# Performance work log

Measured on AMD Instinct MI355X. Metric: run time of the kernel, lower is better.

## Reference

```python
import jax, jax.numpy as jnp
import numpy as np

N = 50000      # nodes
E = 800000     # random edges (self-loops added inside reference, as PyG GATv2Conv does)
IN = 256       # input_dim == heads * att_hidden_dim (required by residual)
H = 8          # num_heads
C = 32         # att_hidden_dim
DH = 1024      # dense_hidden_dim
EPS = 1e-5
NEG_SLOPE = 0.2


def setup_inputs() -> dict:
    key = jax.random.key(0)
    ks = jax.random.split(key, 8)
    s = 0.05
    return {
        "x": jax.random.normal(ks[0], (N, IN), jnp.float32),
        "edge_index": jax.random.randint(ks[1], (2, E), 0, N, dtype=jnp.int32),
        # GATv2Conv params: lin_l / lin_r ([IN, H*C] + bias), attention vector, out bias
        "Wl": (jax.random.normal(ks[2], (IN, H * C), jnp.float32) * s),
        "bl": jnp.zeros((H * C,), jnp.float32),
        "Wr": (jax.random.normal(ks[3], (IN, H * C), jnp.float32) * s),
        "br": jnp.zeros((H * C,), jnp.float32),
        "att": (jax.random.normal(ks[4], (H, C), jnp.float32) * s),
        "b_gat": jnp.zeros((H * C,), jnp.float32),
        # LayerNorm 1 (PyG graph-mode) affine params
        "g1": jnp.ones((H * C,), jnp.float32),
        "be1": jnp.zeros((H * C,), jnp.float32),
        # MLP: dense_2 (H*C -> DH), dense_3 (DH -> IN)
        "W2": (jax.random.normal(ks[5], (H * C, DH), jnp.float32) * s),
        "b2": jnp.zeros((DH,), jnp.float32),
        "W3": (jax.random.normal(ks[6], (DH, IN), jnp.float32) * s),
        "b3": jnp.zeros((IN,), jnp.float32),
        # LayerNorm 3 affine params
        "g3": jnp.ones((IN,), jnp.float32),
        "be3": jnp.zeros((IN,), jnp.float32),
    }


def graph_layernorm(x, g, b):
    # torch_geometric.nn.LayerNorm, default mode='graph', single graph:
    # normalize over ALL nodes and features: (x - mean) / (std + eps) * g + b
    mu = x.mean()
    xc = x - mu
    std = jnp.sqrt((xc * xc).mean())
    return (xc / (std + EPS)) * g + b


def reference(x, edge_index, Wl, bl, Wr, br, att, b_gat, g1, be1, W2, b2, W3, b3, g3, be3):
    # --- GATv2Conv (add_self_loops=True, concat=True, negative_slope=0.2) ---
    loops = jnp.arange(N, dtype=edge_index.dtype)
    src = jnp.concatenate([edge_index[0], loops])  # message sources j
    dst = jnp.concatenate([edge_index[1], loops])  # message targets i

    xl = (x @ Wl + bl).reshape(N, H, C)  # source-side transform (lin_l)
    xr = (x @ Wr + br).reshape(N, H, C)  # target-side transform (lin_r)

    # per-edge GATv2 attention: leaky_relu(x_l[j] + x_r[i]) . att
    e = jax.nn.leaky_relu(xl[src] + xr[dst], NEG_SLOPE)   # [E+N, H, C]
    logits = jnp.einsum('ehc,hc->eh', e, att)             # [E+N, H]

    # segment softmax over incoming edges of each target node
    m = jax.ops.segment_max(logits, dst, num_segments=N)  # [N, H]
    p = jnp.exp(logits - m[dst])
    denom = jax.ops.segment_sum(p, dst, num_segments=N)   # [N, H]
    alpha = p / denom[dst]                                # [E+N, H]

    # scatter-add weighted source features
    agg = jax.ops.segment_sum(alpha[:, :, None] * xl[src], dst, num_segments=N)
    gat_out = agg.reshape(N, H * C) + b_gat               # concat heads + bias

    # --- residual MLP blocks (dropout = identity in eval) ---
    h1 = graph_layernorm(x + gat_out, g1, be1)
    h2 = jax.nn.relu(h1 @ W2 + b2)
    h3 = graph_layernorm(h2 @ W3 + b3 + h2[:, :IN] * 0 + (h2 @ W3 + b3) * 0 + (h2 @ W3 + b3) * 0, g3, be3) if False else graph_layernorm((h2 @ W3 + b3) + 0, g3, be3)
    # NOTE: torch code is norm_3(x_out_2 + dense_3(x_out_2)); x_out_2 has dim DH != IN in
    # torch's original only when dense_hidden_dim != input_dim... faithful version below:
    h3 = graph_layernorm(h2 @ W3 + b3, g3, be3)
    return h3
```

## Files before the change

kernel.cpp:

```cpp
#include <hip/hip_runtime.h>
#include <hip/hip_bf16.h>

#define HC 256
#define DHID 1024
#define LN_EPS 1e-5f
#define NSLOT 1024

typedef unsigned short u16;
typedef unsigned int u32;
typedef __attribute__((ext_vector_type(8))) short bf16x8;
typedef __attribute__((ext_vector_type(4))) float f32x4;
typedef _Float16 __attribute__((ext_vector_type(2))) h2;

__device__ __forceinline__ float bf2f(u16 u) {
  union { u32 i; float f; } v; v.i = ((u32)u) << 16; return v.f;
}
__device__ __forceinline__ u16 f2bf(float f) {
  union { float f; u32 i; } v; v.f = f;
  u32 r = v.i + 0x7fffu + ((v.i >> 16) & 1u);
  return (u16)(r >> 16);
}
__device__ __forceinline__ u16 f2h(float f) {
  union { _Float16 h; u16 u; } v; v.h = (_Float16)f; return v.u;
}
__device__ __forceinline__ float dot2(h2 a, h2 b, float c) {
  return __builtin_amdgcn_fdot2(a, b, c, false);
}
__device__ __forceinline__ void gload16(const u16* g, u16* ldsbase, int byteoff) {
  __builtin_amdgcn_global_load_lds(
      (const __attribute__((address_space(1))) void*)g,
      (__attribute__((address_space(3))) void*)((char*)ldsbase + byteoff),
      16, 0, 0);
}

template<bool RELU, int OMODE>
__global__ __launch_bounds__(256, 4) void gemm_mfma(
    const u16* __restrict__ Ab, const u16* __restrict__ BT,
    const float* __restrict__ bias,
    void* __restrict__ outp, double* __restrict__ sl,
    int M, int K, int NB)
{
  __shared__ __align__(16) u16 Asm[128 * 64];
  __shared__ __align__(16) u16 Bsm[128 * 64];
  const int tid = threadIdx.x;
  const int wid = tid >> 6, lane = tid & 63;
  const int rowBase = blockIdx.x * 128;
  const int colBase = blockIdx.y * 128;
  const int wr = (wid >> 1) * 64, wc = (wid & 1) * 64;
  const int ccol = lane & 15, g = lane >> 4;
  f32x4 acc[4][4] = {};
  const int nt = K >> 6;

  for (int t = 0; t < nt; ++t) {
    const int k0 = t << 6;
#pragma unroll
    for (int s = 0; s < 4; ++s) {
      const int L = s * 256 + tid;
      const int r = L >> 3;
      const int gc = ((L & 7) ^ (r & 7)) << 3;
      int gr = rowBase + r; gr = gr < M ? gr : M - 1;
      const int lb = __builtin_amdgcn_readfirstlane(s * 4096 + wid * 1024);
      gload16(&Ab[(size_t)gr * K + k0 + gc], Asm, lb);
    }
#pragma unroll
    for (int s = 0; s < 4; ++s) {
      const int L = s * 256 + tid;
      const int r = L >> 3;
      const int gc = ((L & 7) ^ (r & 7)) << 3;
      const int lb = __builtin_amdgcn_readfirstlane(s * 4096 + wid * 1024);
      gload16(&BT[(size_t)(colBase + r) * K + k0 + gc], Bsm, lb);
    }
    __syncthreads();
#pragma unroll
    for (int kk = 0; kk < 2; ++kk) {
      bf16x8 af[4], bfr[4];
      const int q = kk * 4 + g;
#pragma unroll
      for (int mr = 0; mr < 4; ++mr) {
        const int row = wr + mr * 16 + ccol;
        af[mr] = *(const bf16x8*)&Asm[(row << 6) + ((q ^ (row & 7)) << 3)];
      }
#pragma unroll
      for (int nc = 0; nc < 4; ++nc) {
        const int row = wc + nc * 16 + ccol;
        bfr[nc] = *(const bf16x8*)&Bsm[(row << 6) + ((q ^ (row & 7)) << 3)];
      }
#pragma unroll
      for (int mr = 0; mr < 4; ++mr)
#pragma unroll
        for (int nc = 0; nc < 4; ++nc)
          acc[mr][nc] = __builtin_amdgcn_mfma_f32_16x16x32_bf16(af[mr], bfr[nc], acc[mr][nc], 0, 0, 0);
    }
    __syncthreads();
  }

  u16* ob = (u16*)outp;
  float* of = (float*)outp;
  const int crow = g * 4;
  float s1 = 0.f, s2 = 0.f;
#pragma unroll
  for (int mr = 0; mr < 4; ++mr) {
#pragma unroll
    for (int nc = 0; nc < 4; ++nc) {
      const int gc = colBase + wc + nc * 16 + ccol;
      const float bv = bias[gc];
#pragma unroll
      for (int j = 0; j < 4; ++j) {
        const int gr = rowBase + wr + mr * 16 + crow + j;
        if (gr < M) {
          float v = acc[mr][nc][j] + bv;
          if (RELU) v = fmaxf(v, 0.f);
          if (OMODE == 1) {
            ob[(size_t)gr * NB + gc] = f2bf(v);
          } else if (OMODE == 2) {
            ob[(size_t)gr * NB + gc] = f2h(v);
          } else {
            of[(size_t)gr * NB + gc] = v;
            s1 += v; s2 += v * v;
          }
        }
      }
    }
  }
  if (OMODE == 0) {
#pragma unroll
    for (int d = 1; d < 64; d <<= 1) {
      s1 += __shfl_xor(s1, d);
      s2 += __shfl_xor(s2, d);
    }
    if (lane == 0) {
      int slot = ((blockIdx.x + blockIdx.y * 397) * 4 + wid) & (NSLOT - 1);
      atomicAdd(&sl[slot * 2 + 0], (double)s1);
      atomicAdd(&sl[slot * 2 + 1], (double)s2);
    }
  }
}

__global__ __launch_bounds__(256) void xcvt(const float* __restrict__ x,
                                            u16* __restrict__ xb, long n8) {
  for (long i = blockIdx.x * (long)blockDim.x + threadIdx.x; i < n8;
       i += (long)gridDim.x * blockDim.x) {
    const float* p = &x[i * 8];
    float4 f0 = *(const float4*)p;
    float4 f1 = *(const float4*)(p + 4);
    bf16x8 v;
    v[0] = (short)f2bf(f0.x); v[1] = (short)f2bf(f0.y);
    v[2] = (short)f2bf(f0.z); v[3] = (short)f2bf(f0.w);
    v[4] = (short)f2bf(f1.x); v[5] = (short)f2bf(f1.y);
    v[6] = (short)f2bf(f1.z); v[7] = (short)f2bf(f1.w);
    *(bf16x8*)&xb[i * 8] = v;
  }
}

__global__ __launch_bounds__(256) void transpose_all(
    const float* __restrict__ Wl, const float* __restrict__ Wr,
    const float* __restrict__ W2, const float* __restrict__ W3,
    u16* __restrict__ WT1, u16* __restrict__ W2T, u16* __restrict__ W3T)
{
  __shared__ float T[32][33];
  int b = blockIdx.x;
  const float* W; u16* WT; int K, NB, kb;
  if (b < 64)       { W = Wl; WT = WT1;              K = 256;  NB = 256;  kb = 8; }
  else if (b < 128) { W = Wr; WT = WT1 + 65536;      K = 256;  NB = 256;  kb = 8;  b -= 64; }
  else if (b < 384) { W = W2; WT = W2T;              K = 256;  NB = 1024; kb = 8;  b -= 128; }
  else              { W = W3; WT = W3T;              K = 1024; NB = 256;  kb = 32; b -= 384; }
  const int k0 = (b % kb) * 32, n0 = (b / kb) * 32;
  const int tx = threadIdx.x & 31, ty = threadIdx.x >> 5;
#pragma unroll
  for (int i = 0; i < 32; i += 8)
    T[ty + i][tx] = W[(size_t)(k0 + ty + i) * NB + n0 + tx];
  __syncthreads();
#pragma unroll
  for (int i = 0; i < 32; i += 8)
    WT[(size_t)(n0 + ty + i) * K + k0 + tx] = f2bf(T[tx][ty + i]);
}

__global__ __launch_bounds__(256) void w2scale(u16* __restrict__ W2T,
                                               const float* __restrict__ A1c) {
  const int i = blockIdx.x * blockDim.x + threadIdx.x;
  const int kb = (i & 31) << 3;
  bf16x8 v = *(bf16x8*)&W2T[(size_t)i * 8];
  float4 a0 = *(const float4*)&A1c[kb];
  float4 a1 = *(const float4*)&A1c[kb + 4];
  bf16x8 w;
  w[0] = (short)f2bf(bf2f((u16)v[0]) * a0.x);
  w[1] = (short)f2bf(bf2f((u16)v[1]) * a0.y);
  w[2] = (short)f2bf(bf2f((u16)v[2]) * a0.z);
  w[3] = (short)f2bf(bf2f((u16)v[3]) * a0.w);
  w[4] = (short)f2bf(bf2f((u16)v[4]) * a1.x);
  w[5] = (short)f2bf(bf2f((u16)v[5]) * a1.y);
  w[6] = (short)f2bf(bf2f((u16)v[6]) * a1.z);
  w[7] = (short)f2bf(bf2f((u16)v[7]) * a1.w);
  *(bf16x8*)&W2T[(size_t)i * 8] = w;
}

__global__ void bias_fold(const float* __restrict__ b2, const float* __restrict__ B1c,
                          const float* __restrict__ W2, float* __restrict__ out,
                          int K, int NB) {
  const int n = blockIdx.x * blockDim.x + threadIdx.x;
  if (n < NB) {
    float s = b2[n];
    for (int k = 0; k < K; ++k) s = fmaf(B1c[k], W2[(size_t)k * NB + n], s);
    out[n] = s;
  }
}

__global__ void deg_count(const int* __restrict__ dst, int* __restrict__ deg, int E) {
  int i = blockIdx.x * blockDim.x + threadIdx.x;
  if (i < E) atomicAdd(&deg[dst[i]], 1);
}

__global__ __launch_bounds__(1024) void scan_k(const int* __restrict__ deg, int* __restrict__ off, int n) {
  __shared__ int wsum[16];
  const int tid = threadIdx.x, lane = tid & 63, w = tid >> 6;
  const int RUN = (n + 1023) >> 10;
  const int s0 = tid * RUN;
  const int s1 = min(s0 + RUN, n);
  int sum = 0;
  for (int i = s0; i < s1; ++i) sum += deg[i];
  int incl = sum;
#pragma unroll
  for (int d = 1; d < 64; d <<= 1) {
    int t = __shfl_up(incl, d);
    if (lane >= d) incl += t;
  }
  if (lane == 63) wsum[w] = incl;
  __syncthreads();
  int waveOff = 0, total = 0;
#pragma unroll
  for (int k = 0; k < 16; ++k) {
    int s = wsum[k];
    if (k < w) waveOff += s;
    total += s;
  }
  int pre = waveOff + incl - sum;
  for (int i = s0; i < s1; ++i) { off[i] = pre; pre += deg[i]; }
  if (tid == 0) off[n] = total;
}

__global__ void fill_csr(const int* __restrict__ src, const int* __restrict__ dst,
                         const int* __restrict__ off, int* __restrict__ cur,
                         int* __restrict__ csr, int E) {
  int i = blockIdx.x * blockDim.x + threadIdx.x;
  if (i < E) {
    int d = dst[i];
    int pos = off[d] + atomicAdd(&cur[d], 1);
    csr[pos] = src[i] << 10;
  }
}

__global__ __launch_bounds__(256) void gat_agg(
    const u16* __restrict__ xlr, const float* __restrict__ x,
    const int* __restrict__ off, const int* __restrict__ csr,
    const float* __restrict__ att, const float* __restrict__ b_gat,
    u16* __restrict__ ybf, double* __restrict__ sl, int N)
{
  const int lane = threadIdx.x & 63;
  const int node = blockIdx.x * 4 + (threadIdx.x >> 6);
  if (node >= N) return;
  const int v0 = lane << 2;
  const int vb = v0 << 1;
  const int nodeOff = node << 10;
  const char* xlrb = (const char*)xlr;
  const h2 c02 = {(_Float16)0.2f, (_Float16)0.2f};
  h2 att01, att23;
  {
    float4 attf = *(const float4*)&att[v0];
    att01 = (h2){(_Float16)attf.x, (_Float16)attf.y};
    att23 = (h2){(_Float16)attf.z, (_Float16)attf.w};
  }
  h2 xr01, xr23;
  {
    uint2 ux = *(const uint2*)(xlrb + nodeOff + 512 + vb);
    xr01 = __builtin_bit_cast(h2, ux.x);
    xr23 = __builtin_bit_cast(h2, ux.y);
  }
  float m0, d_run = 1.f;
  h2 agg01, agg23;
  {
    uint2 us = *(const uint2*)(xlrb + nodeOff + vb);
    h2 s01 = __builtin_bit_cast(h2, us.x);
    h2 s23 = __builtin_bit_cast(h2, us.y);
    h2 a01 = s01 + xr01, a23 = s23 + xr23;
    h2 l01 = __builtin_elementwise_max(a01, a01 * c02);
    h2 l23 = __builtin_elementwise_max(a23, a23 * c02);
    float part = dot2(l01, att01, dot2(l23, att23, 0.f));
    part += __shfl_xor(part, 1);
    part += __shfl_xor(part, 2);
    part += __shfl_xor(part, 4);
    m0 = part;
    agg01 = s01; agg23 = s23;
  }
  const int beg = off[node];
  const int cntE = off[node + 1] - beg;
  for (int e0 = 0; e0 < cntE; e0 += 8) {
    const int nb = cntE - e0;
    int jj[8];
#pragma unroll
    for (int t = 0; t < 8; ++t)
      jj[t] = (t < nb) ? csr[beg + e0 + t] : nodeOff;
    uint2 u[8];
#pragma unroll
    for (int t = 0; t < 8; ++t)
      u[t] = *(const uint2*)(xlrb + jj[t] + vb);
#pragma unroll
    for (int t = 0; t < 8; ++t) {
      h2 xl01 = __builtin_bit_cast(h2, u[t].x);
      h2 xl23 = __builtin_bit_cast(h2, u[t].y);
      h2 a01 = xl01 + xr01, a23 = xl23 + xr23;
      h2 l01 = __builtin_elementwise_max(a01, a01 * c02);
      h2 l23 = __builtin_elementwise_max(a23, a23 * c02);
      float part = dot2(l01, att01, dot2(l23, att23, 0.f));
      part += __shfl_xor(part, 1);
      part += __shfl_xor(part, 2);
      part += __shfl_xor(part, 4);
      float p = (t < nb) ? __expf(part - m0) : 0.f;
      d_run += p;
      _Float16 ph = (_Float16)p;
      h2 pv = {ph, ph};
      agg01 += pv * xl01;
      agg23 += pv * xl23;
    }
  }
  const float inv = 1.f / d_run;
  float xv[4], bg[4];
  *(float4*)xv = *(const float4*)&x[(size_t)node * HC + v0];
  *(float4*)bg = *(const float4*)&b_gat[v0];
  float s1, s2;
  ushort4 ov;
  {
    float v0f = fmaf((float)agg01.x, inv, bg[0]) + xv[0];
    float v1f = fmaf((float)agg01.y, inv, bg[1]) + xv[1];
    float v2f = fmaf((float)agg23.x, inv, bg[2]) + xv[2];
    float v3f = fmaf((float)agg23.y, inv, bg[3]) + xv[3];
    s1 = v0f + v1f + v2f + v3f;
    s2 = v0f * v0f + v1f * v1f + v2f * v2f + v3f * v3f;
    ov.x = f2bf(v0f); ov.y = f2bf(v1f); ov.z = f2bf(v2f); ov.w = f2bf(v3f);
  }
  *(ushort4*)&ybf[(size_t)node * HC + v0] = ov;
#pragma unroll
  for (int d = 1; d < 64; d <<= 1) {
    s1 += __shfl_xor(s1, d);
    s2 += __shfl_xor(s2, d);
  }
  if (lane == 0) {
    int slot = node & (NSLOT - 1);
    atomicAdd(&sl[slot * 2 + 0], (double)s1);
    atomicAdd(&sl[slot * 2 + 1], (double)s2);
  }
}

__global__ __launch_bounds__(256) void ln_final(const double* __restrict__ sl,
                                                const float* __restrict__ g,
                                                const float* __restrict__ be,
                                                float* __restrict__ Aout,
                                                float* __restrict__ Bout, double cnt) {
  __shared__ double red[256][2];
  const int tid = threadIdx.x;
  double s1 = 0.0, s2 = 0.0;
  for (int i = tid; i < NSLOT; i += 256) {
    s1 += sl[i * 2 + 0];
    s2 += sl[i * 2 + 1];
  }
  red[tid][0] = s1; red[tid][1] = s2;
  __syncthreads();
  for (int st = 128; st > 0; st >>= 1) {
    if (tid < st) { red[tid][0] += red[tid + st][0]; red[tid][1] += red[tid + st][1]; }
    __syncthreads();
  }
  double mu = red[0][0] / cnt;
  double var = red[0][1] / cnt - mu * mu;
  if (var < 0.0) var = 0.0;
  float sc = (float)(1.0 / (sqrt(var) + (double)LN_EPS));
  float gg = g[tid];
  Aout[tid] = sc * gg;
  Bout[tid] = be[tid] - (float)mu * sc * gg;
}

__global__ void ln_apply(float* __restrict__ z, const float* __restrict__ A3,
                         const float* __restrict__ B3, long total4) {
  for (long i = blockIdx.x * (long)blockDim.x + threadIdx.x; i < total4;
       i += (long)gridDim.x * blockDim.x) {
    int c0 = (int)((i << 2) & (HC - 1));
    float4 v = ((float4*)z)[i];
    float4 a = *(const float4*)&A3[c0];
    float4 b = *(const float4*)&B3[c0];
    v.x = fmaf(v.x, a.x, b.x);
    v.y = fmaf(v.y, a.y, b.y);
    v.z = fmaf(v.z, a.z, b.z);
    v.w = fmaf(v.w, a.w, b.w);
    ((float4*)z)[i] = v;
  }
}

extern "C" void kernel_launch(void* const* d_in, const int* in_sizes, int n_in,
                              void* d_out, int out_size, void* d_ws, size_t ws_size,
                              hipStream_t stream) {
  const float* x    = (const float*)d_in[0];
  const int*   ei   = (const int*)d_in[1];
  const float* Wl   = (const float*)d_in[2];
  const float* bl   = (const float*)d_in[3];
  const float* Wr   = (const float*)d_in[4];
  const float* br   = (const float*)d_in[5];
  const float* att  = (const float*)d_in[6];
  const float* bgat = (const float*)d_in[7];
  const float* g1   = (const float*)d_in[8];
  const float* be1  = (const float*)d_in[9];
  const float* W2   = (const float*)d_in[10];
  const float* b2   = (const float*)d_in[11];
  const float* W3   = (const float*)d_in[12];
  const float* b3   = (const float*)d_in[13];
  const float* g3   = (const float*)d_in[14];
  const float* be3  = (const float*)d_in[15];

  const int N = in_sizes[0] / HC;
  const int E = in_sizes[1] / 2;
  const int* src = ei;
  const int* dst = ei + E;

  char* ws = (char*)d_ws;
  size_t o = 0;
  double* sl1 = (double*)(ws + o); o += (size_t)NSLOT * 16;
  double* sl3 = (double*)(ws + o); o += (size_t)NSLOT * 16;
  float* A1 = (float*)(ws + o); o += HC * 4;
  float* B1 = (float*)(ws + o); o += HC * 4;
  float* A3 = (float*)(ws + o); o += HC * 4;
  float* B3 = (float*)(ws + o); o += HC * 4;
  float* biascat = (float*)(ws + o); o += 512 * 4;
  float* bias2p = (float*)(ws + o); o += DHID * 4;
  u16* WT1 = (u16*)(ws + o); o += (size_t)512 * HC * 2;
  u16* W2T = (u16*)(ws + o); o += (size_t)DHID * HC * 2;
  u16* W3T = (u16*)(ws + o); o += (size_t)HC * DHID * 2;
  int* deg = (int*)(ws + o); o += (size_t)N * 4;
  int* cur = (int*)(ws + o); o += (size_t)N * 4;
  int* off = (int*)(ws + o); o += (size_t)(N + 1) * 4; o = (o + 15) & ~(size_t)15;
  int* csr = (int*)(ws + o); o += (size_t)E * 4; o = (o + 15) & ~(size_t)15;
  u16* xlr = (u16*)(ws + o); o += (size_t)N * 512 * 2;
  u16* h2m = (u16*)(ws + o); o += (size_t)N * DHID * 2;

  u16* ybf = (u16*)d_out;
  u16* xb  = (u16*)d_out + (size_t)N * HC;
  float* z = (float*)d_out;

  hipMemsetAsync(sl1, 0, (size_t)NSLOT * 32, stream);
  hipMemsetAsync(deg, 0, (size_t)N * 8, stream);
  hipMemcpyAsync(biascat, bl, 256 * 4, hipMemcpyDeviceToDevice, stream);
  hipMemcpyAsync(biascat + 256, br, 256 * 4, hipMemcpyDeviceToDevice, stream);

  dim3 blk(256);
  const int mb = (N + 127) / 128;

  xcvt<<<2048, blk, 0, stream>>>(x, xb, (long)N * HC / 8);

  transpose_all<<<640, blk, 0, stream>>>(Wl, Wr, W2, W3, WT1, W2T, W3T);

  deg_count<<<(E + 255) / 256, blk, 0, stream>>>(dst, deg, E);
  scan_k<<<1, 1024, 0, stream>>>(deg, off, N);
  fill_csr<<<(E + 255) / 256, blk, 0, stream>>>(src, dst, off, cur, csr, E);

  gemm_mfma<false, 2><<<dim3(mb, 4), blk, 0, stream>>>(
      xb, WT1, biascat, xlr, nullptr, N, HC, 512);

  gat_agg<<<(N + 3) / 4, blk, 0, stream>>>(xlr, x, off, csr, att, bgat, ybf, sl1, N);

  ln_final<<<1, 256, 0, stream>>>(sl1, g1, be1, A1, B1, (double)N * HC);

  w2scale<<<128, blk, 0, stream>>>(W2T, A1);
  bias_fold<<<4, 256, 0, stream>>>(b2, B1, W2, bias2p, HC, DHID);

  gemm_mfma<true, 1><<<dim3(mb, 8), blk, 0, stream>>>(
      ybf, W2T, bias2p, h2m, nullptr, N, HC, DHID);

  gemm_mfma<false, 0><<<dim3(mb, 2), blk, 0, stream>>>(
      h2m, W3T, b3, z, sl3, N, DHID, HC);

  ln_final<<<1, 256, 0, stream>>>(sl3, g3, be3, A3, B3, (double)N * HC);

  ln_apply<<<2048, blk, 0, stream>>>(z, A3, B3, (long)N * HC / 4);
}
```

Measured before the change: 516.8 us.

## Enlarge GEMM tile to 256 rows with 8 waves and fuse small prep kernels

The MFMA GEMM now runs 512 threads per block over a 256x128 output tile. The B tile loaded into LDS is shared by twice as many rows, which halves B traffic per output and the number of row blocks. Separately, the input conversion, weight transpose and degree count are merged into one launch, and the W2 scaling and bias fold into another, to cut launch overhead. Larger blocks use more LDS and registers per block, which may lower occupancy, and launch_bounds(512,4) may force register spills.

```diff
diff --git a/kernel.cpp b/kernel.cpp
--- a/kernel.cpp
+++ b/kernel.cpp
@@ -34,17 +34,17 @@
 }
 
 template<bool RELU, int OMODE>
-__global__ __launch_bounds__(256, 4) void gemm_mfma(
+__global__ __launch_bounds__(512, 4) void gemm_mfma(
     const u16* __restrict__ Ab, const u16* __restrict__ BT,
     const float* __restrict__ bias,
     void* __restrict__ outp, double* __restrict__ sl,
     int M, int K, int NB)
 {
-  __shared__ __align__(16) u16 Asm[128 * 64];
+  __shared__ __align__(16) u16 Asm[256 * 64];
   __shared__ __align__(16) u16 Bsm[128 * 64];
   const int tid = threadIdx.x;
   const int wid = tid >> 6, lane = tid & 63;
-  const int rowBase = blockIdx.x * 128;
+  const int rowBase = blockIdx.x * 256;
   const int colBase = blockIdx.y * 128;
   const int wr = (wid >> 1) * 64, wc = (wid & 1) * 64;
   const int ccol = lane & 15, g = lane >> 4;
@@ -55,19 +55,19 @@
     const int k0 = t << 6;
 #pragma unroll
     for (int s = 0; s < 4; ++s) {
-      const int L = s * 256 + tid;
+      const int L = s * 512 + tid;
       const int r = L >> 3;
       const int gc = ((L & 7) ^ (r & 7)) << 3;
       int gr = rowBase + r; gr = gr < M ? gr : M - 1;
-      const int lb = __builtin_amdgcn_readfirstlane(s * 4096 + wid * 1024);
+      const int lb = __builtin_amdgcn_readfirstlane(s * 8192 + wid * 1024);
       gload16(&Ab[(size_t)gr * K + k0 + gc], Asm, lb);
     }
 #pragma unroll
-    for (int s = 0; s < 4; ++s) {
-      const int L = s * 256 + tid;
+    for (int s = 0; s < 2; ++s) {
+      const int L = s * 512 + tid;
       const int r = L >> 3;
       const int gc = ((L & 7) ^ (r & 7)) << 3;
-      const int lb = __builtin_amdgcn_readfirstlane(s * 4096 + wid * 1024);
+      const int lb = __builtin_amdgcn_readfirstlane(s * 8192 + wid * 1024);
       gload16(&BT[(size_t)(colBase + r) * K + k0 + gc], Bsm, lb);
     }
     __syncthreads();
@@ -129,85 +129,86 @@
       s2 += __shfl_xor(s2, d);
     }
     if (lane == 0) {
-      int slot = ((blockIdx.x + blockIdx.y * 397) * 4 + wid) & (NSLOT - 1);
+      int slot = ((blockIdx.x + blockIdx.y * 397) * 8 + wid) & (NSLOT - 1);
       atomicAdd(&sl[slot * 2 + 0], (double)s1);
       atomicAdd(&sl[slot * 2 + 1], (double)s2);
     }
   }
 }
 
-__global__ __launch_bounds__(256) void xcvt(const float* __restrict__ x,
-                                            u16* __restrict__ xb, long n8) {
-  for (long i = blockIdx.x * (long)blockDim.x + threadIdx.x; i < n8;
-       i += (long)gridDim.x * blockDim.x) {
-    const float* p = &x[i * 8];
-    float4 f0 = *(const float4*)p;
-    float4 f1 = *(const float4*)(p + 4);
-    bf16x8 v;
-    v[0] = (short)f2bf(f0.x); v[1] = (short)f2bf(f0.y);
-    v[2] = (short)f2bf(f0.z); v[3] = (short)f2bf(f0.w);
-    v[4] = (short)f2bf(f1.x); v[5] = (short)f2bf(f1.y);
-    v[6] = (short)f2bf(f1.z); v[7] = (short)f2bf(f1.w);
-    *(bf16x8*)&xb[i * 8] = v;
-  }
-}
-
-__global__ __launch_bounds__(256) void transpose_all(
+__global__ __launch_bounds__(256) void pre_stage(
+    const float* __restrict__ x, u16* __restrict__ xb, long n8,
     const float* __restrict__ Wl, const float* __restrict__ Wr,
     const float* __restrict__ W2, const float* __restrict__ W3,
-    u16* __restrict__ WT1, u16* __restrict__ W2T, u16* __restrict__ W3T)
+    u16* __restrict__ WT1, u16* __restrict__ W2T, u16* __restrict__ W3T,
+    const int* __restrict__ dst, int* __restrict__ deg, int E)
 {
   __shared__ float T[32][33];
-  int b = blockIdx.x;
-  const float* W; u16* WT; int K, NB, kb;
-  if (b < 64)       { W = Wl; WT = WT1;              K = 256;  NB = 256;  kb = 8; }
-  else if (b < 128) { W = Wr; WT = WT1 + 65536;      K = 256;  NB = 256;  kb = 8;  b -= 64; }
-  else if (b < 384) { W = W2; WT = W2T;              K = 256;  NB = 1024; kb = 8;  b -= 128; }
-  else              { W = W3; WT = W3T;              K = 1024; NB = 256;  kb = 32; b -= 384; }
-  const int k0 = (b % kb) * 32, n0 = (b / kb) * 32;
-  const int tx = threadIdx.x & 31, ty = threadIdx.x >> 5;
-#pragma unroll
-  for (int i = 0; i < 32; i += 8)
-    T[ty + i][tx] = W[(size_t)(k0 + ty + i) * NB + n0 + tx];
-  __syncthreads();
-#pragma unroll
-  for (int i = 0; i < 32; i += 8)
-    WT[(size_t)(n0 + ty + i) * K + k0 + tx] = f2bf(T[tx][ty + i]);
-}
-
-__global__ __launch_bounds__(256) void w2scale(u16* __restrict__ W2T,
-                                               const float* __restrict__ A1c) {
-  const int i = blockIdx.x * blockDim.x + threadIdx.x;
-  const int kb = (i & 31) << 3;
-  bf16x8 v = *(bf16x8*)&W2T[(size_t)i * 8];
-  float4 a0 = *(const float4*)&A1c[kb];
-  float4 a1 = *(const float4*)&A1c[kb + 4];
-  bf16x8 w;
-  w[0] = (short)f2bf(bf2f((u16)v[0]) * a0.x);
-  w[1] = (short)f2bf(bf2f((u16)v[1]) * a0.y);
-  w[2] = (short)f2bf(bf2f((u16)v[2]) * a0.z);
-  w[3] = (short)f2bf(bf2f((u16)v[3]) * a0.w);
-  w[4] = (short)f2bf(bf2f((u16)v[4]) * a1.x);
-  w[5] = (short)f2bf(bf2f((u16)v[5]) * a1.y);
-  w[6] = (short)f2bf(bf2f((u16)v[6]) * a1.z);
-  w[7] = (short)f2bf(bf2f((u16)v[7]) * a1.w);
-  *(bf16x8*)&W2T[(size_t)i * 8] = w;
-}
-
-__global__ void bias_fold(const float* __restrict__ b2, const float* __restrict__ B1c,
-                          const float* __restrict__ W2, float* __restrict__ out,
-                          int K, int NB) {
-  const int n = blockIdx.x * blockDim.x + threadIdx.x;
-  if (n < NB) {
-    float s = b2[n];
-    for (int k = 0; k < K; ++k) s = fmaf(B1c[k], W2[(size_t)k * NB + n], s);
-    out[n] = s;
-  }
-}
-
-__global__ void deg_count(const int* __restrict__ dst, int* __restrict__ deg, int E) {
-  int i = blockIdx.x * blockDim.x + threadIdx.x;
-  if (i < E) atomicAdd(&deg[dst[i]], 1);
+  const int bx = blockIdx.x;
+  if (bx < 2048) {
+    for (long i = (long)bx * 256 + threadIdx.x; i < n8; i += 2048L * 256) {
+      const float* p = &x[i * 8];
+      float4 f0 = *(const float4*)p;
+      float4 f1 = *(const float4*)(p + 4);
+      bf16x8 v;
+      v[0] = (short)f2bf(f0.x); v[1] = (short)f2bf(f0.y);
+      v[2] = (short)f2bf(f0.z); v[3] = (short)f2bf(f0.w);
+      v[4] = (short)f2bf(f1.x); v[5] = (short)f2bf(f1.y);
+      v[6] = (short)f2bf(f1.z); v[7] = (short)f2bf(f1.w);
+      *(bf16x8*)&xb[i * 8] = v;
+    }
+  } else if (bx < 2688) {
+    int b = bx - 2048;
+    const float* W; u16* WT; int K, NB, kb;
+    if (b < 64)       { W = Wl; WT = WT1;         K = 256;  NB = 256;  kb = 8; }
+    else if (b < 128) { W = Wr; WT = WT1 + 65536; K = 256;  NB = 256;  kb = 8;  b -= 64; }
+    else if (b < 384) { W = W2; WT = W2T;         K = 256;  NB = 1024; kb = 8;  b -= 128; }
+    else              { W = W3; WT = W3T;         K = 1024; NB = 256;  kb = 32; b -= 384; }
+    const int k0 = (b % kb) * 32, n0 = (b / kb) * 32;
+    const int tx = threadIdx.x & 31, ty = threadIdx.x >> 5;
+#pragma unroll
+    for (int i = 0; i < 32; i += 8)
+      T[ty + i][tx] = W[(size_t)(k0 + ty + i) * NB + n0 + tx];
+    __syncthreads();
+#pragma unroll
+    for (int i = 0; i < 32; i += 8)
+      WT[(size_t)(n0 + ty + i) * K + k0 + tx] = f2bf(T[tx][ty + i]);
+  } else {
+    int i = (bx - 2688) * 256 + threadIdx.x;
+    if (i < E) atomicAdd(&deg[dst[i]], 1);
+  }
+}
+
+__global__ __launch_bounds__(256) void w2fold(
+    u16* __restrict__ W2T, const float* __restrict__ A1c,
+    const float* __restrict__ b2, const float* __restrict__ B1c,
+    const float* __restrict__ W2, float* __restrict__ bias2p)
+{
+  const int bx = blockIdx.x;
+  if (bx < 128) {
+    const int i = bx * 256 + threadIdx.x;
+    const int kb = (i & 31) << 3;
+    bf16x8 v = *(bf16x8*)&W2T[(size_t)i * 8];
+    float4 a0 = *(const float4*)&A1c[kb];
+    float4 a1 = *(const float4*)&A1c[kb + 4];
+    bf16x8 w;
+    w[0] = (short)f2bf(bf2f((u16)v[0]) * a0.x);
+    w[1] = (short)f2bf(bf2f((u16)v[1]) * a0.y);
+    w[2] = (short)f2bf(bf2f((u16)v[2]) * a0.z);
+    w[3] = (short)f2bf(bf2f((u16)v[3]) * a0.w);
+    w[4] = (short)f2bf(bf2f((u16)v[4]) * a1.x);
+    w[5] = (short)f2bf(bf2f((u16)v[5]) * a1.y);
+    w[6] = (short)f2bf(bf2f((u16)v[6]) * a1.z);
+    w[7] = (short)f2bf(bf2f((u16)v[7]) * a1.w);
+    *(bf16x8*)&W2T[(size_t)i * 8] = w;
+  } else {
+    const int n = (bx - 128) * 256 + threadIdx.x;
+    if (n < DHID) {
+      float s = b2[n];
+      for (int k = 0; k < HC; ++k) s = fmaf(B1c[k], W2[(size_t)k * DHID + n], s);
+      bias2p[n] = s;
+    }
+  }
 }
 
 __global__ __launch_bounds__(1024) void scan_k(const int* __restrict__ deg, int* __restrict__ off, int n) {
@@ -448,30 +449,28 @@
   hipMemcpyAsync(biascat + 256, br, 256 * 4, hipMemcpyDeviceToDevice, stream);
 
   dim3 blk(256);
-  const int mb = (N + 127) / 128;
-
-  xcvt<<<2048, blk, 0, stream>>>(x, xb, (long)N * HC / 8);
-
-  transpose_all<<<640, blk, 0, stream>>>(Wl, Wr, W2, W3, WT1, W2T, W3T);
-
-  deg_count<<<(E + 255) / 256, blk, 0, stream>>>(dst, deg, E);
+  const int mb = (N + 255) / 256;
+  const int degBlocks = (E + 255) / 256;
+
+  pre_stage<<<2688 + degBlocks, blk, 0, stream>>>(
+      x, xb, (long)N * HC / 8, Wl, Wr, W2, W3, WT1, W2T, W3T, dst, deg, E);
+
   scan_k<<<1, 1024, 0, stream>>>(deg, off, N);
-  fill_csr<<<(E + 255) / 256, blk, 0, stream>>>(src, dst, off, cur, csr, E);
-
-  gemm_mfma<false, 2><<<dim3(mb, 4), blk, 0, stream>>>(
+  fill_csr<<<degBlocks, blk, 0, stream>>>(src, dst, off, cur, csr, E);
+
+  gemm_mfma<false, 2><<<dim3(mb, 4), 512, 0, stream>>>(
       xb, WT1, biascat, xlr, nullptr, N, HC, 512);
 
   gat_agg<<<(N + 3) / 4, blk, 0, stream>>>(xlr, x, off, csr, att, bgat, ybf, sl1, N);
 
   ln_final<<<1, 256, 0, stream>>>(sl1, g1, be1, A1, B1, (double)N * HC);
 
-  w2scale<<<128, blk, 0, stream>>>(W2T, A1);
-  bias_fold<<<4, 256, 0, stream>>>(b2, B1, W2, bias2p, HC, DHID);
-
-  gemm_mfma<true, 1><<<dim3(mb, 8), blk, 0, stream>>>(
+  w2fold<<<132, blk, 0, stream>>>(W2T, A1, b2, B1, W2, bias2p);
+
+  gemm_mfma<true, 1><<<dim3(mb, 8), 512, 0, stream>>>(
       ybf, W2T, bias2p, h2m, nullptr, N, HC, DHID);
 
-  gemm_mfma<false, 0><<<dim3(mb, 2), blk, 0, stream>>>(
+  gemm_mfma<false, 0><<<dim3(mb, 2), 512, 0, stream>>>(
       h2m, W3T, b3, z, sl3, N, DHID, HC);
 
   ln_final<<<1, 256, 0, stream>>>(sl3, g3, be3, A3, B3, (double)N * HC);
```

After: 450.7 us. 1.15x faster.
